# Performance work log

Measured on AMD Instinct MI355X. Metric: run time of the kernel, lower is better.

Reference implementation:

```python
import jax, jax.numpy as jnp
import numpy as np

TOTAL_LABELS = 21
TOTAL_POS_BBOXES = 64


def _make_boxes(key, batch, n):
    # valid [y1,x1,y2,x2] boxes in [0,1]
    k1, k2 = jax.random.split(key)
    tl = jax.random.uniform(k1, (batch, n, 2)) * 0.7          # y1, x1
    wh = jax.random.uniform(k2, (batch, n, 2)) * 0.3 + 0.01   # h, w
    br = jnp.minimum(tl + wh, 1.0)                            # y2, x2
    return jnp.concatenate([tl, br], axis=-1).astype(jnp.float32)


def setup_inputs() -> dict:
    key = jax.random.key(0)
    k1, k2, k3 = jax.random.split(key, 3)
    batch, n_roi, n_gt = 32, 2000, 100
    roi_bboxes = _make_boxes(k1, batch, n_roi)
    gt_boxes = _make_boxes(k2, batch, n_gt)
    gt_labels = jax.random.randint(k3, (batch, n_gt), 0, TOTAL_LABELS, dtype=jnp.int32)
    return {"roi_bboxes": roi_bboxes, "gt_boxes": gt_boxes, "gt_labels": gt_labels}


def generate_iou_map(bboxes, gt_boxes):
    # bboxes: (b, n, 4), gt_boxes: (b, m, 4) -> iou: (b, n, m)
    by1, bx1, by2, bx2 = jnp.split(bboxes, 4, axis=-1)        # each (b, n, 1)
    gy1, gx1, gy2, gx2 = jnp.split(gt_boxes, 4, axis=-1)      # each (b, m, 1)
    gt_area = jnp.squeeze((gy2 - gy1) * (gx2 - gx1), axis=-1)  # (b, m)
    bb_area = jnp.squeeze((by2 - by1) * (bx2 - bx1), axis=-1)  # (b, n)
    x_top = jnp.maximum(bx1, jnp.swapaxes(gx1, 1, 2))
    y_top = jnp.maximum(by1, jnp.swapaxes(gy1, 1, 2))
    x_bot = jnp.minimum(bx2, jnp.swapaxes(gx2, 1, 2))
    y_bot = jnp.minimum(by2, jnp.swapaxes(gy2, 1, 2))
    inter = jnp.maximum(x_bot - x_top, 0.0) * jnp.maximum(y_bot - y_top, 0.0)  # (b, n, m)
    union = bb_area[:, :, None] + gt_area[:, None, :] - inter
    return inter / union


def get_deltas_from_bboxes(bboxes, gt_boxes):
    bw = bboxes[..., 3] - bboxes[..., 1]
    bh = bboxes[..., 2] - bboxes[..., 0]
    bcx = bboxes[..., 1] + 0.5 * bw
    bcy = bboxes[..., 0] + 0.5 * bh
    gw = gt_boxes[..., 3] - gt_boxes[..., 1]
    gh = gt_boxes[..., 2] - gt_boxes[..., 0]
    gcx = gt_boxes[..., 1] + 0.5 * gw
    gcy = gt_boxes[..., 0] + 0.5 * gh
    bw = jnp.where(bw == 0, 1e-3, bw)
    bh = jnp.where(bh == 0, 1e-3, bh)
    dx = jnp.where(gw == 0, 0.0, (gcx - bcx) / bw)
    dy = jnp.where(gh == 0, 0.0, (gcy - bcy) / bh)
    dw = jnp.where(gw == 0, 0.0, jnp.log(jnp.where(gw == 0, 1.0, gw / bw)))
    dh = jnp.where(gh == 0, 0.0, jnp.log(jnp.where(gh == 0, 1.0, gh / bh)))
    return jnp.stack([dy, dx, dh, dw], axis=-1)


def reference(roi_bboxes, gt_boxes, gt_labels):
    batch, n_roi = roi_bboxes.shape[0], roi_bboxes.shape[1]
    iou_map = generate_iou_map(roi_bboxes, gt_boxes)                 # (b, n, m)
    max_idx = jnp.argmax(iou_map, axis=2).astype(jnp.int32)          # (b, n)
    merged = jnp.max(iou_map, axis=2)                                # (b, n)
    order = jnp.argsort(-merged, axis=1)                             # descending
    rank = jnp.argsort(order, axis=1)                                # rank of each roi
    pos_mask = rank < TOTAL_POS_BBOXES                               # (b, n)
    gt_boxes_map = jnp.take_along_axis(gt_boxes, max_idx[..., None], axis=1)   # (b, n, 4)
    expanded_gt_boxes = jnp.where(pos_mask[..., None], gt_boxes_map, 0.0)
    gt_labels_map = jnp.take_along_axis(gt_labels, max_idx, axis=1)  # (b, n)
    expanded_gt_labels = jnp.where(pos_mask, gt_labels_map, 0)
    deltas = get_deltas_from_bboxes(roi_bboxes, expanded_gt_boxes)   # (b, n, 4)
    labels = jax.nn.one_hot(expanded_gt_labels, TOTAL_LABELS, dtype=deltas.dtype)  # (b, n, L)
    # per-class delta expansion: (b, n, L, 1) * (b, n, 1, 4) -> (b, n*L, 4)
    roi_bbox_deltas = (labels[..., None] * deltas[:, :, None, :]).reshape(
        batch, n_roi * TOTAL_LABELS, 4)
    return (jax.lax.stop_gradient(roi_bbox_deltas), jax.lax.stop_gradient(labels))
```

## Files before the change

### kernel.cpp

```cpp
#include <hip/hip_runtime.h>

#define BATCH 32
#define NROI  2000
#define NGT   100
#define NLBL  21
#define NPOS  64

typedef float nfloat4 __attribute__((ext_vector_type(4)));

__device__ __forceinline__ void nt_store(const float4& v, float4* p) {
  nfloat4 nv = {v.x, v.y, v.z, v.w};
  __builtin_nontemporal_store(nv, (nfloat4*)p);
}


__global__ __launch_bounds__(256) void iou_max_kernel(
    const float4* __restrict__ roi, const float4* __restrict__ gt,
    unsigned long long* __restrict__ keys, int* __restrict__ maxidx) {
  __shared__ float4 sgt[NGT];
  __shared__ float sga[NGT];
  const int b = blockIdx.y;
  const int r = blockIdx.x * 256 + threadIdx.x;
  if (threadIdx.x < NGT) {
    float4 g = gt[b * NGT + threadIdx.x];
    sgt[threadIdx.x] = g;
    sga[threadIdx.x] = __fmul_rn(__fsub_rn(g.z, g.x), __fsub_rn(g.w, g.y));
  }
  __syncthreads();
  if (r >= NROI) return;
  float4 rb = roi[b * NROI + r];
  float bb_area = __fmul_rn(__fsub_rn(rb.z, rb.x), __fsub_rn(rb.w, rb.y));
  float best = -1.0f;
  int bi = 0;
#pragma unroll 4
  for (int m = 0; m < NGT; ++m) {
    float4 g = sgt[m];
    float xt = fmaxf(rb.y, g.y);
    float yt = fmaxf(rb.x, g.x);
    float xb = fminf(rb.w, g.w);
    float yb = fminf(rb.z, g.z);
    float iw = fmaxf(__fsub_rn(xb, xt), 0.0f);
    float ih = fmaxf(__fsub_rn(yb, yt), 0.0f);
    float inter = __fmul_rn(iw, ih);
    float uni = __fsub_rn(__fadd_rn(bb_area, sga[m]), inter);
    float iou = __fdiv_rn(inter, uni);
    if (iou > best) { best = iou; bi = m; }
  }
  unsigned int fb = __float_as_uint(best);
  keys[b * NROI + r] =
      ((unsigned long long)fb << 16) | (unsigned long long)(0xFFFFu - (unsigned)r);
  maxidx[b * NROI + r] = bi;
}

__global__ __launch_bounds__(256) void select_kernel(
    const unsigned long long* __restrict__ keys, const int* __restrict__ maxidx,
    const float4* __restrict__ gt, const int* __restrict__ gtlab,
    float4* __restrict__ egt, int* __restrict__ lab) {
  const int b = blockIdx.x;
  const int t = threadIdx.x;
  unsigned long long k[8];
#pragma unroll
  for (int j = 0; j < 8; ++j) {
    int i = t + j * 256;
    k[j] = (i < NROI) ? keys[b * NROI + i] : 0ull;
  }
  __shared__ int hist[256];
  __shared__ int wtot[4];
  __shared__ int sbin, sneed;
  unsigned long long prefix = 0;
  int need = NPOS;
  const int lane = t & 63;
#pragma unroll
  for (int p = 0; p < 6; ++p) {
    const int shift = 40 - 8 * p;
    hist[t] = 0;
    __syncthreads();
    const unsigned long long hmask = ~((1ull << (shift + 8)) - 1);
#pragma unroll
    for (int j = 0; j < 8; ++j) {
      if ((k[j] & hmask) == prefix)
        atomicAdd(&hist[(int)((k[j] >> shift) & 255)], 1);
    }
    __syncthreads();
    int v = hist[t];
    int S = v;
#pragma unroll
    for (int off = 1; off < 64; off <<= 1) {
      int u = __shfl_down(S, off, 64);
      if (lane + off < 64) S += u;
    }
    if (lane == 0) wtot[t >> 6] = S;
    __syncthreads();
    int w = t >> 6;
#pragma unroll
    for (int w2 = 1; w2 < 4; ++w2)
      if (w2 > w) S += wtot[w2];
    if (S >= need && (S - v) < need) { sbin = t; sneed = need - (S - v); }
    __syncthreads();
    prefix |= ((unsigned long long)sbin) << shift;
    need = sneed;
  }
  const unsigned long long k64 = prefix;
#pragma unroll
  for (int j = 0; j < 8; ++j) {
    int i = t + j * 256;
    if (i < NROI) {
      int ridx = b * NROI + i;
      float4 g = make_float4(0.f, 0.f, 0.f, 0.f);
      int lb = 0;
      if (k[j] >= k64) {
        int mi = maxidx[ridx];
        g = gt[b * NGT + mi];
        lb = gtlab[b * NGT + mi];
      }
      egt[ridx] = g;
      lab[ridx] = lb;
    }
  }
}

__global__ __launch_bounds__(256) void write_out_kernel(
    const float4* __restrict__ roi, const float4* __restrict__ egt,
    const int* __restrict__ lab, float4* __restrict__ out) {
  const int ND4 = BATCH * NROI * NLBL;
  const int NL4 = (BATCH * NROI * NLBL) / 4;
  int i = blockIdx.x * 256 + threadIdx.x;
  if (i < ND4) {
    int b = i / (NROI * NLBL);
    int rem = i - b * (NROI * NLBL);
    int r = rem / NLBL;
    int cls = rem - r * NLBL;
    int ridx = b * NROI + r;
    float4 v = make_float4(0.f, 0.f, 0.f, 0.f);
    if (cls == lab[ridx]) {
      float4 g = egt[ridx];
      float4 rb = roi[ridx];
      float bw = rb.w - rb.y, bh = rb.z - rb.x;
      float bcx = rb.y + 0.5f * bw, bcy = rb.x + 0.5f * bh;
      float gw = g.w - g.y, gh = g.z - g.x;
      float gcx = g.y + 0.5f * gw, gcy = g.x + 0.5f * gh;
      if (bw == 0.f) bw = 1e-3f;
      if (bh == 0.f) bh = 1e-3f;
      float dx  = (gw == 0.f) ? 0.f : (gcx - bcx) / bw;
      float dy  = (gh == 0.f) ? 0.f : (gcy - bcy) / bh;
      float dwv = (gw == 0.f) ? 0.f : logf(gw / bw);
      float dhv = (gh == 0.f) ? 0.f : logf(gh / bh);
      v = make_float4(dy, dx, dhv, dwv);
    }
    nt_store(v, &out[i]);
  } else if (i < ND4 + NL4) {
    int i2 = i - ND4;
    int e = i2 * 4;
    float v[4];
#pragma unroll
    for (int kk = 0; kk < 4; ++kk) {
      int ei = e + kk;
      int b = ei / (NROI * NLBL);
      int rem = ei - b * (NROI * NLBL);
      int r = rem / NLBL;
      int cls = rem - r * NLBL;
      v[kk] = (cls == lab[b * NROI + r]) ? 1.0f : 0.0f;
    }
    float4 vv = make_float4(v[0], v[1], v[2], v[3]);
    nt_store(vv, &out[i]);
  }
}

extern "C" void kernel_launch(void* const* d_in, const int* in_sizes, int n_in,
                              void* d_out, int out_size, void* d_ws, size_t ws_size,
                              hipStream_t stream) {
  const float* roi = (const float*)d_in[0];
  const float* gt  = (const float*)d_in[1];
  const int* gtlab = (const int*)d_in[2];

  char* ws = (char*)d_ws;
  unsigned long long* keys = (unsigned long long*)ws;
  int*    maxidx = (int*)(ws + 512000);
  float4* egt    = (float4*)(ws + 768000);
  int*    lab    = (int*)(ws + 1792000);

  iou_max_kernel<<<dim3(8, BATCH), 256, 0, stream>>>(
      (const float4*)roi, (const float4*)gt, keys, maxidx);
  select_kernel<<<dim3(BATCH), 256, 0, stream>>>(
      keys, maxidx, (const float4*)gt, gtlab, egt, lab);
  const int total4 = BATCH * NROI * NLBL + (BATCH * NROI * NLBL) / 4;
  write_out_kernel<<<dim3((total4 + 255) / 256), 256, 0, stream>>>(
      (const float4*)roi, egt, lab, (float4*)d_out);
}
```

Measured before the change: 88.61 us.

## Compute per-ROI deltas in IoU kernel and aggregate first radix histogram pass

The box-delta computation and label lookup move into the IoU/argmax kernel, which now writes a per-ROI delta and label. The select kernel only emits a packed positive-label code, and the write-out kernel copies the precomputed delta instead of recomputing it per class element. The first radix-select pass now aggregates histogram counts per wavefront with ballot/shuffle, to cut contention on shared-memory atomics where most keys share a top byte. In exchange, deltas are computed for every ROI rather than only positives, and the ballot loop can iterate many times when digits differ.

Result: no change. 88.56 us (-0.1%).

```diff
diff --git a/kernel.cpp b/kernel.cpp
--- a/kernel.cpp
+++ b/kernel.cpp
@@ -16,15 +16,18 @@
 
 __global__ __launch_bounds__(256) void iou_max_kernel(
     const float4* __restrict__ roi, const float4* __restrict__ gt,
-    unsigned long long* __restrict__ keys, int* __restrict__ maxidx) {
+    const int* __restrict__ gtlab, unsigned long long* __restrict__ keys,
+    float4* __restrict__ delta, int* __restrict__ klab) {
   __shared__ float4 sgt[NGT];
   __shared__ float sga[NGT];
+  __shared__ int sgl[NGT];
   const int b = blockIdx.y;
   const int r = blockIdx.x * 256 + threadIdx.x;
   if (threadIdx.x < NGT) {
     float4 g = gt[b * NGT + threadIdx.x];
     sgt[threadIdx.x] = g;
     sga[threadIdx.x] = __fmul_rn(__fsub_rn(g.z, g.x), __fsub_rn(g.w, g.y));
+    sgl[threadIdx.x] = gtlab[b * NGT + threadIdx.x];
   }
   __syncthreads();
   if (r >= NROI) return;
@@ -46,16 +49,28 @@
     float iou = __fdiv_rn(inter, uni);
     if (iou > best) { best = iou; bi = m; }
   }
+  const int ridx = b * NROI + r;
   unsigned int fb = __float_as_uint(best);
-  keys[b * NROI + r] =
+  keys[ridx] =
       ((unsigned long long)fb << 16) | (unsigned long long)(0xFFFFu - (unsigned)r);
-  maxidx[b * NROI + r] = bi;
+  float4 g = sgt[bi];
+  float bw = rb.w - rb.y, bh = rb.z - rb.x;
+  float bcx = rb.y + 0.5f * bw, bcy = rb.x + 0.5f * bh;
+  float gw = g.w - g.y, gh = g.z - g.x;
+  float gcx = g.y + 0.5f * gw, gcy = g.x + 0.5f * gh;
+  if (bw == 0.f) bw = 1e-3f;
+  if (bh == 0.f) bh = 1e-3f;
+  float dx  = (gw == 0.f) ? 0.f : (gcx - bcx) / bw;
+  float dy  = (gh == 0.f) ? 0.f : (gcy - bcy) / bh;
+  float dwv = (gw == 0.f) ? 0.f : logf(gw / bw);
+  float dhv = (gh == 0.f) ? 0.f : logf(gh / bh);
+  delta[ridx] = make_float4(dy, dx, dhv, dwv);
+  klab[ridx] = sgl[bi];
 }
 
 __global__ __launch_bounds__(256) void select_kernel(
-    const unsigned long long* __restrict__ keys, const int* __restrict__ maxidx,
-    const float4* __restrict__ gt, const int* __restrict__ gtlab,
-    float4* __restrict__ egt, int* __restrict__ lab) {
+    const unsigned long long* __restrict__ keys, const int* __restrict__ klab,
+    int* __restrict__ pc) {
   const int b = blockIdx.x;
   const int t = threadIdx.x;
   unsigned long long k[8];
@@ -75,11 +90,27 @@
     const int shift = 40 - 8 * p;
     hist[t] = 0;
     __syncthreads();
-    const unsigned long long hmask = ~((1ull << (shift + 8)) - 1);
-#pragma unroll
-    for (int j = 0; j < 8; ++j) {
-      if ((k[j] & hmask) == prefix)
-        atomicAdd(&hist[(int)((k[j] >> shift) & 255)], 1);
+    if (p == 0) {
+#pragma unroll
+      for (int j = 0; j < 8; ++j) {
+        unsigned d = (unsigned)((k[j] >> 40) & 255);
+        unsigned long long rem = ~0ull;
+        while (rem) {
+          int leader = __builtin_ctzll(rem);
+          unsigned dl = (unsigned)__shfl((int)d, leader, 64);
+          unsigned long long m = __ballot(d == dl);
+          if (lane == leader)
+            atomicAdd(&hist[dl], (int)__builtin_popcountll(m));
+          rem &= ~m;
+        }
+      }
+    } else {
+      const unsigned long long hmask = ~((1ull << (shift + 8)) - 1);
+#pragma unroll
+      for (int j = 0; j < 8; ++j) {
+        if ((k[j] & hmask) == prefix)
+          atomicAdd(&hist[(int)((k[j] >> shift) & 255)], 1);
+      }
     }
     __syncthreads();
     int v = hist[t];
@@ -106,22 +137,16 @@
     int i = t + j * 256;
     if (i < NROI) {
       int ridx = b * NROI + i;
-      float4 g = make_float4(0.f, 0.f, 0.f, 0.f);
-      int lb = 0;
-      if (k[j] >= k64) {
-        int mi = maxidx[ridx];
-        g = gt[b * NGT + mi];
-        lb = gtlab[b * NGT + mi];
-      }
-      egt[ridx] = g;
-      lab[ridx] = lb;
+      int v = 0;
+      if (k[j] >= k64) v = klab[ridx] + 1;
+      pc[ridx] = v;
     }
   }
 }
 
 __global__ __launch_bounds__(256) void write_out_kernel(
-    const float4* __restrict__ roi, const float4* __restrict__ egt,
-    const int* __restrict__ lab, float4* __restrict__ out) {
+    const int* __restrict__ pc, const float4* __restrict__ delta,
+    float4* __restrict__ out) {
   const int ND4 = BATCH * NROI * NLBL;
   const int NL4 = (BATCH * NROI * NLBL) / 4;
   int i = blockIdx.x * 256 + threadIdx.x;
@@ -130,23 +155,9 @@
     int rem = i - b * (NROI * NLBL);
     int r = rem / NLBL;
     int cls = rem - r * NLBL;
-    int ridx = b * NROI + r;
+    int p = pc[b * NROI + r];
     float4 v = make_float4(0.f, 0.f, 0.f, 0.f);
-    if (cls == lab[ridx]) {
-      float4 g = egt[ridx];
-      float4 rb = roi[ridx];
-      float bw = rb.w - rb.y, bh = rb.z - rb.x;
-      float bcx = rb.y + 0.5f * bw, bcy = rb.x + 0.5f * bh;
-      float gw = g.w - g.y, gh = g.z - g.x;
-      float gcx = g.y + 0.5f * gw, gcy = g.x + 0.5f * gh;
-      if (bw == 0.f) bw = 1e-3f;
-      if (bh == 0.f) bh = 1e-3f;
-      float dx  = (gw == 0.f) ? 0.f : (gcx - bcx) / bw;
-      float dy  = (gh == 0.f) ? 0.f : (gcy - bcy) / bh;
-      float dwv = (gw == 0.f) ? 0.f : logf(gw / bw);
-      float dhv = (gh == 0.f) ? 0.f : logf(gh / bh);
-      v = make_float4(dy, dx, dhv, dwv);
-    }
+    if (cls + 1 == p) v = delta[b * NROI + r];
     nt_store(v, &out[i]);
   } else if (i < ND4 + NL4) {
     int i2 = i - ND4;
@@ -159,7 +170,9 @@
       int rem = ei - b * (NROI * NLBL);
       int r = rem / NLBL;
       int cls = rem - r * NLBL;
-      v[kk] = (cls == lab[b * NROI + r]) ? 1.0f : 0.0f;
+      int p = pc[b * NROI + r];
+      int lc = (p != 0) ? (p - 1) : 0;
+      v[kk] = (cls == lc) ? 1.0f : 0.0f;
     }
     float4 vv = make_float4(v[0], v[1], v[2], v[3]);
     nt_store(vv, &out[i]);
@@ -175,15 +188,14 @@
 
   char* ws = (char*)d_ws;
   unsigned long long* keys = (unsigned long long*)ws;
-  int*    maxidx = (int*)(ws + 512000);
-  float4* egt    = (float4*)(ws + 768000);
-  int*    lab    = (int*)(ws + 1792000);
+  float4* delta = (float4*)(ws + 512000);
+  int*    klab  = (int*)(ws + 1536000);
+  int*    pc    = (int*)(ws + 1792000);
 
   iou_max_kernel<<<dim3(8, BATCH), 256, 0, stream>>>(
-      (const float4*)roi, (const float4*)gt, keys, maxidx);
-  select_kernel<<<dim3(BATCH), 256, 0, stream>>>(
-      keys, maxidx, (const float4*)gt, gtlab, egt, lab);
+      (const float4*)roi, (const float4*)gt, gtlab, keys, delta, klab);
+  select_kernel<<<dim3(BATCH), 256, 0, stream>>>(keys, klab, pc);
   const int total4 = BATCH * NROI * NLBL + (BATCH * NROI * NLBL) / 4;
   write_out_kernel<<<dim3((total4 + 255) / 256), 256, 0, stream>>>(
-      (const float4*)roi, egt, lab, (float4*)d_out);
-}
+      pc, delta, (float4*)d_out);
+}
```
